# Kernel tuning notes

Measured on AMD Instinct MI355X. Metric: run time of the kernel, lower is better.

Reference implementation:

```python
import jax, jax.numpy as jnp
import numpy as np

N_EXPERTS = 8
TOPK = 2
W_IMPORTANCE = 0.01
W_LOAD = 0.01
LAMBDA_Z = 0.001
W_PENALTY = 0.01
PENALTY_TEMP = 1.66


def setup_inputs() -> dict:
    key = jax.random.key(0)
    ks = jax.random.split(key, 8)
    B, S, D, H, E = 8, 4096, 512, 2048, N_EXPERTS
    T = B * S
    return {
        "x": jax.random.normal(ks[0], (B, S, D), dtype=jnp.float32),
        "gate_w": jax.random.normal(ks[1], (E, D), dtype=jnp.float32) * 0.02,
        "noise_w": jax.random.normal(ks[2], (E, D), dtype=jnp.float32) * 0.02,
        "bias": jnp.zeros((E,), dtype=jnp.float32),
        "c_fc_w": jax.random.normal(ks[3], (E, H, D), dtype=jnp.float32) * 0.02,
        "c_fc_b": jnp.zeros((E, H), dtype=jnp.float32),
        "c_proj_w": jax.random.normal(ks[4], (E, D, H), dtype=jnp.float32) * 0.02,
        "c_proj_b": jnp.zeros((E, D), dtype=jnp.float32),
        "noise": jax.random.normal(ks[5], (T, E), dtype=jnp.float32),
    }


def reference(x, gate_w, noise_w, bias, c_fc_w, c_fc_b, c_proj_w, c_proj_b, noise):
    E, K = N_EXPERTS, TOPK
    D = x.shape[-1]
    xs = x.reshape(-1, D)                      # [T, D]
    T = xs.shape[0]

    gate_logits = xs @ gate_w.T                # [T, E]

    # penalty (pre-noise logits)
    p = jax.nn.softmax(gate_logits / PENALTY_TEMP, axis=-1)
    penalty_a = jnp.mean(p * (1.0 - p))
    pm = p.mean(axis=0)
    penalty_b = 1.0 / E - jnp.mean(pm * (1.0 - pm))
    penalty = (penalty_a + penalty_b) * W_PENALTY

    # z-loss (pre-noise logits)
    lse = jax.scipy.special.logsumexp(gate_logits, axis=-1)
    z_loss = LAMBDA_Z * jnp.mean(lse ** 2)

    # noisy gating + bias
    noise_std = jax.nn.softplus(xs @ noise_w.T)
    gate_logits = gate_logits + noise * noise_std + bias

    weights_vals, selected = jax.lax.top_k(gate_logits, K)   # [T, K]
    weights = jax.nn.softmax(weights_vals.astype(jnp.float32), axis=1).astype(x.dtype)

    # importance loss: scatter-add weights per expert
    importance = jax.ops.segment_sum(weights.reshape(-1), selected.reshape(-1),
                                     num_segments=E)
    cv2 = jnp.var(importance) / jnp.mean(importance) ** 2
    importance_loss = W_IMPORTANCE * cv2

    # load loss: top-1 counts vs mean router probs (post-noise)
    router_probs = jax.nn.softmax(gate_logits.astype(jnp.float32), axis=-1).astype(x.dtype)
    top1 = selected[:, 0]
    fi = jax.ops.segment_sum(jnp.ones((T,), dtype=jnp.float32), top1,
                             num_segments=E) / T
    load_loss = W_LOAD * E * jnp.sum(fi * router_probs.mean(axis=0))

    aux = penalty + z_loss + importance_loss + load_loss

    # combine weights per (token, expert): [T, E]
    comb = jnp.zeros((T, E), dtype=x.dtype).at[jnp.arange(T)[:, None], selected].add(weights)

    results = jnp.zeros_like(xs)
    for e in range(E):  # fixed small expert count
        h = jax.nn.gelu(xs @ c_fc_w[e].T + c_fc_b[e], approximate=True)
        o = h @ c_proj_w[e].T + c_proj_b[e]
        results = results + comb[:, e:e + 1] * o

    return results.reshape(x.shape), aux
```

## Files before the change

### kernel.cpp

```cpp
#include <hip/hip_runtime.h>
#include <hip/hip_bf16.h>
#include <stdint.h>

#define TTOK 32768
#define DDIM 512
#define HDIM 2048
#define NEXP 8
#define SBLK 128
#define IDXS (TTOK + 256)

typedef __attribute__((ext_vector_type(4))) float f32x4;
typedef __attribute__((ext_vector_type(8))) short bf16x8;

#define GLOAD16(gp, lp)                                                      \
  __builtin_amdgcn_global_load_lds(                                          \
      (const __attribute__((address_space(1))) unsigned int*)(gp),           \
      (__attribute__((address_space(3))) unsigned int*)(lp), 16, 0, 0)

__device__ __forceinline__ ushort f2bf(float f) {
  union { float f; uint32_t u; } cv; cv.f = f;
  uint32_t u = cv.u;
  u = u + 0x7fffu + ((u >> 16) & 1u);
  return (ushort)(u >> 16);
}

__device__ __forceinline__ float bf2f(ushort u) {
  union { uint32_t u; float f; } cv; cv.u = ((uint32_t)u) << 16;
  return cv.f;
}

__device__ __forceinline__ float gelu_fast(float v) {
  float y = 1.5957691216057308f * (v + 0.044715f * v * v * v);
  return v / (1.0f + __expf(-y));
}

__global__ __launch_bounds__(256) void cvtw2_kernel(
    const float* __restrict__ srcA, const float* __restrict__ srcB,
    ushort* __restrict__ dstA, ushort* __restrict__ dstB, int n4each) {
  int i = blockIdx.x * blockDim.x + threadIdx.x;
  const float* s;
  ushort* d;
  int j;
  if (i < n4each) { s = srcA; d = dstA; j = i; }
  else { j = i - n4each; if (j >= n4each) return; s = srcB; d = dstB; }
  float4 v = reinterpret_cast<const float4*>(s)[j];
  ushort4 o;
  o.x = f2bf(v.x); o.y = f2bf(v.y); o.z = f2bf(v.z); o.w = f2bf(v.w);
  reinterpret_cast<ushort4*>(d)[j] = o;
}

__global__ __launch_bounds__(256, 2) void gating1_kernel(
    const float* __restrict__ x, const float* __restrict__ gw,
    const float* __restrict__ nw, ushort* __restrict__ xbf,
    float* __restrict__ logits) {
  __shared__ float xs[16][516];
  __shared__ float wsm[16][516];
  const int tid = threadIdx.x;
  const int t0 = blockIdx.x * 16;

  for (int i = tid; i < 2048; i += 256) {
    int row = i >> 7;
    int d4 = (i & 127) << 2;
    const float* src = (row < 8) ? (gw + row * DDIM + d4)
                                 : (nw + (row - 8) * DDIM + d4);
    *reinterpret_cast<float4*>(&wsm[row][d4]) =
        *reinterpret_cast<const float4*>(src);
  }
  for (int i = tid; i < 2048; i += 256) {
    int row = i >> 7;
    int d4 = (i & 127) << 2;
    float4 v = *reinterpret_cast<const float4*>(x + (size_t)(t0 + row) * DDIM + d4);
    *reinterpret_cast<float4*>(&xs[row][d4]) = v;
    ushort4 u;
    u.x = f2bf(v.x); u.y = f2bf(v.y); u.z = f2bf(v.z); u.w = f2bf(v.w);
    *reinterpret_cast<ushort4*>(xbf + (size_t)(t0 + row) * DDIM + d4) = u;
  }
  __syncthreads();

  const int unit = tid & 15;
  const int tok = tid >> 4;
  const float* xr = &xs[tok][0];
  const float* wr = &wsm[unit][0];
  float a0 = 0.f, a1 = 0.f, a2 = 0.f, a3 = 0.f;
#pragma unroll 16
  for (int d = 0; d < 512; d += 4) {
    float4 xv = *reinterpret_cast<const float4*>(xr + d);
    float4 wv = *reinterpret_cast<const float4*>(wr + d);
    a0 = fmaf(xv.x, wv.x, a0);
    a1 = fmaf(xv.y, wv.y, a1);
    a2 = fmaf(xv.z, wv.z, a2);
    a3 = fmaf(xv.w, wv.w, a3);
  }
  logits[(size_t)(t0 + tok) * 16 + unit] = (a0 + a1) + (a2 + a3);
}

__global__ void gating2_kernel(
    const float* __restrict__ logits, const float* __restrict__ noise,
    const float* __restrict__ bias, int* __restrict__ cnt,
    int* __restrict__ idxl, int2* __restrict__ slots,
    float2* __restrict__ tokw, float* __restrict__ part) {
  const int tid = threadIdx.x;
  const int lane = tid & 63, wave = tid >> 6;
  const int t = blockIdx.x * 256 + tid;

  const float4* lp = reinterpret_cast<const float4*>(logits + (size_t)t * 16);
  float4 l0 = lp[0], l1 = lp[1], l2 = lp[2], l3 = lp[3];
  float lg[NEXP] = {l0.x, l0.y, l0.z, l0.w, l1.x, l1.y, l1.z, l1.w};
  float nl[NEXP] = {l2.x, l2.y, l2.z, l2.w, l3.x, l3.y, l3.z, l3.w};
  const float4* np = reinterpret_cast<const float4*>(noise + (size_t)t * NEXP);
  float4 z0 = np[0], z1 = np[1];
  float nz[NEXP] = {z0.x, z0.y, z0.z, z0.w, z1.x, z1.y, z1.z, z1.w};
  float bia[NEXP];
#pragma unroll
  for (int e = 0; e < NEXP; ++e) bia[e] = bias[e];

  float pa = 0.f, pm[NEXP];
  {
    float sv[NEXP];
#pragma unroll
    for (int e = 0; e < NEXP; ++e) sv[e] = lg[e] * (1.0f / 1.66f);
    float mx = sv[0];
#pragma unroll
    for (int e = 1; e < NEXP; ++e) mx = fmaxf(mx, sv[e]);
    float ssum = 0.f, pv[NEXP];
#pragma unroll
    for (int e = 0; e < NEXP; ++e) { pv[e] = __expf(sv[e] - mx); ssum += pv[e]; }
    float sinv = 1.f / ssum;
#pragma unroll
    for (int e = 0; e < NEXP; ++e) {
      float pe = pv[e] * sinv;
      pa += pe * (1.f - pe);
      pm[e] = pe;
    }
  }
  float z2;
  {
    float mg = lg[0];
#pragma unroll
    for (int e = 1; e < NEXP; ++e) mg = fmaxf(mg, lg[e]);
    float es = 0.f;
#pragma unroll
    for (int e = 0; e < NEXP; ++e) es += __expf(lg[e] - mg);
    float lse = mg + __logf(es);
    z2 = lse * lse;
  }
  float g2[NEXP];
#pragma unroll
  for (int e = 0; e < NEXP; ++e) {
    float s = nl[e];
    float sp = fmaxf(s, 0.f) + __logf(1.f + __expf(-fabsf(s)));
    g2[e] = lg[e] + nz[e] * sp + bia[e];
  }
  float v1 = g2[0]; int i1 = 0;
#pragma unroll
  for (int e = 1; e < NEXP; ++e) if (g2[e] > v1) { v1 = g2[e]; i1 = e; }
  float v2 = -3.4e38f; int i2 = 0;
#pragma unroll
  for (int e = 0; e < NEXP; ++e) if (e != i1 && g2[e] > v2) { v2 = g2[e]; i2 = e; }
  float dd = __expf(v2 - v1);
  float w1 = 1.f / (1.f + dd);
  float w2 = dd / (1.f + dd);
  float rp[NEXP];
  {
    float mr = g2[0];
#pragma unroll
    for (int e = 1; e < NEXP; ++e) mr = fmaxf(mr, g2[e]);
    float rs = 0.f, er[NEXP];
#pragma unroll
    for (int e = 0; e < NEXP; ++e) { er[e] = __expf(g2[e] - mr); rs += er[e]; }
    float rinv = 1.f / rs;
#pragma unroll
    for (int e = 0; e < NEXP; ++e) rp[e] = er[e] * rinv;
  }

  float loc[34];
  loc[0] = pa; loc[1] = z2;
#pragma unroll
  for (int e = 0; e < NEXP; ++e) {
    loc[2 + e]  = pm[e];
    loc[10 + e] = (e == i1 ? w1 : 0.f) + (e == i2 ? w2 : 0.f);
    loc[18 + e] = rp[e];
    loc[26 + e] = (e == i1) ? 1.f : 0.f;
  }
#pragma unroll
  for (int m = 1; m < 64; m <<= 1) {
#pragma unroll
    for (int s = 0; s < 34; ++s) loc[s] += __shfl_xor(loc[s], m);
  }
  __shared__ float red[4][34];
  if (lane == 0) {
#pragma unroll
    for (int s = 0; s < 34; ++s) red[wave][s] = loc[s];
  }
  __shared__ int lcnt[NEXP], gbase[NEXP];
  if (tid < NEXP) lcnt[tid] = 0;
  __syncthreads();
  int p1 = atomicAdd(&lcnt[i1], 1);
  int p2 = atomicAdd(&lcnt[i2], 1);
  __syncthreads();
  if (tid < NEXP) gbase[tid] = atomicAdd(&cnt[tid], lcnt[tid]);
  if (tid < 34) {
    float s = red[0][tid] + red[1][tid] + red[2][tid] + red[3][tid];
    part[(size_t)tid * SBLK + blockIdx.x] = s;
  }
  __syncthreads();
  int q1 = gbase[i1] + p1, q2 = gbase[i2] + p2;
  idxl[i1 * IDXS + q1] = t;
  idxl[i2 * IDXS + q2] = t;
  slots[t] = make_int2((i1 << 16) | q1, (i2 << 16) | q2);
  tokw[t] = make_float2(w1, w2);
}

__global__ __launch_bounds__(256) void finalize_kernel(
    const float* __restrict__ part, const int* __restrict__ cnt,
    int* __restrict__ offs, int* __restrict__ idxl,
    float* __restrict__ aux_out) {
  __shared__ float sums[34];
  __shared__ float red[4][34];
  __shared__ int roundc[NEXP], base[NEXP];
  const int tid = threadIdx.x;
  const int lane = tid & 63, wave = tid >> 6;

  float loc[34];
#pragma unroll
  for (int s = 0; s < 34; ++s) loc[s] = 0.f;
  for (int b = tid; b < SBLK; b += 256) {
#pragma unroll
    for (int s = 0; s < 34; ++s) loc[s] += part[(size_t)s * SBLK + b];
  }
#pragma unroll
  for (int m = 1; m < 64; m <<= 1) {
#pragma unroll
    for (int s = 0; s < 34; ++s) loc[s] += __shfl_xor(loc[s], m);
  }
  if (lane == 0) {
#pragma unroll
    for (int s = 0; s < 34; ++s) red[wave][s] = loc[s];
  }
  if (tid == 0) {
    int acc = 0;
    for (int e = 0; e < NEXP; ++e) {
      int r = (cnt[e] + 255) & ~255;
      roundc[e] = r; base[e] = acc; acc += r;
    }
  }
  __syncthreads();
  if (tid < 34) sums[tid] = red[0][tid] + red[1][tid] + red[2][tid] + red[3][tid];
  __syncthreads();
  for (int i = tid; i < NEXP * 256; i += 256) {
    int e = i >> 8, k = i & 255;
    int pos = cnt[e] + k;
    if (pos < roundc[e]) idxl[e * IDXS + pos] = 0;
  }
  if (tid < NEXP) offs[tid] = base[tid];
  if (tid == 0) {
    const float Tf = (float)TTOK;
    float pa = sums[0] / (Tf * 8.f);
    float pbm = 0.f;
    for (int e = 0; e < NEXP; ++e) { float pm = sums[2 + e] / Tf; pbm += pm * (1.f - pm); }
    float pb = 1.f / 8.f - pbm / 8.f;
    float penalty = (pa + pb) * 0.01f;
    float z = 0.001f * sums[1] / Tf;
    float mean = 0.f;
    for (int e = 0; e < NEXP; ++e) mean += sums[10 + e];
    mean /= 8.f;
    float var = 0.f;
    for (int e = 0; e < NEXP; ++e) { float d = sums[10 + e] - mean; var += d * d; }
    var /= 8.f;
    float il = 0.01f * var / (mean * mean);
    float ld = 0.f;
    for (int e = 0; e < NEXP; ++e) ld += (sums[26 + e] / Tf) * (sums[18 + e] / Tf);
    ld *= 0.01f * 8.f;
    aux_out[0] = penalty + z + il + ld;
  }
}


__global__ __launch_bounds__(512, 4) void gemm1_kernel(
    const ushort* __restrict__ xbf, const ushort* __restrict__ wfc,
    const float* __restrict__ fcb, const int* __restrict__ idxl,
    const int* __restrict__ cnt, const int* __restrict__ offs,
    ushort* __restrict__ h, int hbase, int HC) {
  const int e = blockIdx.z;
  const int count = cnt[e];
  const int rounded = (count + 255) & ~255;
  const int mt = blockIdx.x;
  if (mt * 256 >= rounded) return;
  const int nt = blockIdx.y;
  const int tid = threadIdx.x;
  const int lane = tid & 63, wave = tid >> 6;
  const int wm = wave >> 1, wn = wave & 1;

  __shared__ ushort As[256][64];
  __shared__ ushort Bs[128][64];

  const int srow = tid >> 3;
  const int csw8 = (((tid & 7) ^ (srow & 7)) << 3);
  const int dst8 = ((tid & 7) << 3);

  const ushort* aptr[4];
#pragma unroll
  for (int r = 0; r < 4; ++r) {
    int g = idxl[e * IDXS + mt * 256 + srow + r * 64];
    aptr[r] = xbf + (size_t)g * DDIM + csw8;
  }
  const ushort* bptr = wfc + (size_t)e * (HDIM * DDIM) +
                       (size_t)(hbase + nt * 128 + srow) * DDIM + csw8;

  f32x4 acc[4][4];
#pragma unroll
  for (int m = 0; m < 4; ++m)
#pragma unroll
    for (int n = 0; n < 4; ++n)
      acc[m][n] = (f32x4){0.f, 0.f, 0.f, 0.f};

  const int NK = DDIM / 64;
  for (int kt = 0; kt < NK; ++kt) {
    const int koff = kt * 64;
#pragma unroll
    for (int r = 0; r < 4; ++r)
      GLOAD16(aptr[r] + koff, &As[srow + r * 64][dst8]);
#pragma unroll
    for (int r = 0; r < 2; ++r)
      GLOAD16(bptr + (size_t)(r * 64) * DDIM + koff, &Bs[srow + r * 64][dst8]);
    asm volatile("s_waitcnt vmcnt(0)" ::: "memory");
    __syncthreads();
#pragma unroll
    for (int ks = 0; ks < 2; ++ks) {
      const int ch = (((ks << 2) | (lane >> 4)) ^ (lane & 7)) << 3;
      bf16x8 af[4], bfr[4];
#pragma unroll
      for (int m = 0; m < 4; ++m)
        af[m] = *reinterpret_cast<const bf16x8*>(&As[wm * 64 + m * 16 + (lane & 15)][ch]);
#pragma unroll
      for (int n = 0; n < 4; ++n)
        bfr[n] = *reinterpret_cast<const bf16x8*>(&Bs[wn * 64 + n * 16 + (lane & 15)][ch]);
#pragma unroll
      for (int m = 0; m < 4; ++m)
#pragma unroll
        for (int n = 0; n < 4; ++n)
          acc[m][n] = __builtin_amdgcn_mfma_f32_16x16x32_bf16(af[m], bfr[n], acc[m][n], 0, 0, 0);
    }
    __syncthreads();
  }

  const int hb = offs[e];
#pragma unroll
  for (int n = 0; n < 4; ++n) {
    const int col = wn * 64 + n * 16 + (lane & 15);
    const int gcol = hbase + nt * 128 + col;
    const float bterm = fcb[e * HDIM + gcol];
#pragma unroll
    for (int m = 0; m < 4; ++m) {
#pragma unroll
      for (int j = 0; j < 4; ++j) {
        const int row = mt * 256 + wm * 64 + m * 16 + ((lane >> 4) << 2) + j;
        float v = acc[m][n][j] + bterm;
        h[(size_t)(hb + row) * HC + (nt * 128 + col)] = f2bf(gelu_fast(v));
      }
    }
  }
}

__global__ __launch_bounds__(512, 4) void gemm2_kernel(
    const ushort* __restrict__ h, const ushort* __restrict__ wpj,
    const float* __restrict__ pjb, const int* __restrict__ cnt,
    const int* __restrict__ offs, ushort* __restrict__ scratch,
    int hbase, int HC, int first_chunk) {
  const int e = blockIdx.z;
  const int count = cnt[e];
  const int rounded = (count + 255) & ~255;
  const int mt = blockIdx.x;
  if (mt * 256 >= rounded) return;
  const int nt = blockIdx.y;
  const int tid = threadIdx.x;
  const int lane = tid & 63, wave = tid >> 6;
  const int wm = wave >> 1, wn = wave & 1;

  __shared__ ushort As[256][64];
  __shared__ ushort Bs[128][64];

  const int srow = tid >> 3;
  const int csw8 = (((tid & 7) ^ (srow & 7)) << 3);
  const int dst8 = ((tid & 7) << 3);
  const int hb = offs[e];

  const ushort* abase = h + (size_t)(hb + mt * 256 + srow) * HC + csw8;
  const ushort* bbase = wpj + (size_t)e * (DDIM * HDIM) +
                        (size_t)(nt * 128 + srow) * HDIM + hbase + csw8;

  f32x4 acc[4][4];
#pragma unroll
  for (int m = 0; m < 4; ++m)
#pragma unroll
    for (int n = 0; n < 4; ++n)
      acc[m][n] = (f32x4){0.f, 0.f, 0.f, 0.f};

  const int NK = HC / 64;
  for (int kt = 0; kt < NK; ++kt) {
    const int koff = kt * 64;
#pragma unroll
    for (int r = 0; r < 4; ++r)
      GLOAD16(abase + (size_t)(r * 64) * HC + koff, &As[srow + r * 64][dst8]);
#pragma unroll
    for (int r = 0; r < 2; ++r)
      GLOAD16(bbase + (size_t)(r * 64) * HDIM + koff, &Bs[srow + r * 64][dst8]);
    asm volatile("s_waitcnt vmcnt(0)" ::: "memory");
    __syncthreads();
#pragma unroll
    for (int ks = 0; ks < 2; ++ks) {
      const int ch = (((ks << 2) | (lane >> 4)) ^ (lane & 7)) << 3;
      bf16x8 af[4], bfr[4];
#pragma unroll
      for (int m = 0; m < 4; ++m)
        af[m] = *reinterpret_cast<const bf16x8*>(&As[wm * 64 + m * 16 + (lane & 15)][ch]);
#pragma unroll
      for (int n = 0; n < 4; ++n)
        bfr[n] = *reinterpret_cast<const bf16x8*>(&Bs[wn * 64 + n * 16 + (lane & 15)][ch]);
#pragma unroll
      for (int m = 0; m < 4; ++m)
#pragma unroll
        for (int n = 0; n < 4; ++n)
          acc[m][n] = __builtin_amdgcn_mfma_f32_16x16x32_bf16(af[m], bfr[n], acc[m][n], 0, 0, 0);
    }
    __syncthreads();
  }

#pragma unroll
  for (int n = 0; n < 4; ++n) {
    const int col = nt * 128 + wn * 64 + n * 16 + (lane & 15);
    const float bterm = pjb[e * DDIM + col];
#pragma unroll
    for (int m = 0; m < 4; ++m) {
#pragma unroll
      for (int j = 0; j < 4; ++j) {
        const size_t row = (size_t)(hb + mt * 256 + wm * 64 + m * 16 + ((lane >> 4) << 2) + j);
        ushort* p = scratch + row * DDIM + col;
        float v = acc[m][n][j];
        if (first_chunk) v += bterm;
        else v += bf2f(*p);
        *p = f2bf(v);
      }
    }
  }
}

__global__ __launch_bounds__(256, 8) void combine_kernel(
    const ushort* __restrict__ scratch, const int* __restrict__ offs,
    const int2* __restrict__ slots, const float2* __restrict__ tokw,
    float* __restrict__ out) {
  const int lane = threadIdx.x & 63;
  const int wave = threadIdx.x >> 6;
  const int t = blockIdx.x * 4 + wave;
  int2 s = slots[t];
  float2 w = tokw[t];
  const int r1 = offs[s.x >> 16] + (s.x & 0xFFFF);
  const int r2 = offs[s.y >> 16] + (s.y & 0xFFFF);
  bf16x8 a = *reinterpret_cast<const bf16x8*>(scratch + (size_t)r1 * DDIM + lane * 8);
  bf16x8 b = *reinterpret_cast<const bf16x8*>(scratch + (size_t)r2 * DDIM + lane * 8);
  float r[8];
#pragma unroll
  for (int j = 0; j < 8; ++j)
    r[j] = w.x * bf2f((ushort)a[j]) + w.y * bf2f((ushort)b[j]);
  float4* op = reinterpret_cast<float4*>(out + (size_t)t * DDIM + lane * 8);
  op[0] = make_float4(r[0], r[1], r[2], r[3]);
  op[1] = make_float4(r[4], r[5], r[6], r[7]);
}

extern "C" void kernel_launch(void* const* d_in, const int* in_sizes, int n_in,
                              void* d_out, int out_size, void* d_ws, size_t ws_size,
                              hipStream_t stream) {
  const float* x    = (const float*)d_in[0];
  const float* gw   = (const float*)d_in[1];
  const float* nw   = (const float*)d_in[2];
  const float* bias = (const float*)d_in[3];
  const float* fcw  = (const float*)d_in[4];
  const float* fcb  = (const float*)d_in[5];
  const float* pjw  = (const float*)d_in[6];
  const float* pjb  = (const float*)d_in[7];
  const float* noise = (const float*)d_in[8];
  float* out = (float*)d_out;

  char* ws = (char*)d_ws;
  size_t o = 0;
  auto alloc = [&](size_t bytes) -> char* {
    char* p = ws + o;
    o += (bytes + 255) & ~(size_t)255;
    return p;
  };
  ushort* xbf    = (ushort*)alloc((size_t)TTOK * DDIM * 2);
  ushort* wfcb   = (ushort*)alloc((size_t)NEXP * HDIM * DDIM * 2);
  ushort* wpjb   = (ushort*)alloc((size_t)NEXP * DDIM * HDIM * 2);
  float*  logits = (float*)alloc((size_t)TTOK * 16 * 4);
  int*    idxl   = (int*)alloc((size_t)NEXP * IDXS * 4);
  int2*   slots  = (int2*)alloc((size_t)TTOK * 8);
  float2* tokw   = (float2*)alloc((size_t)TTOK * 8);
  int*    cnt    = (int*)alloc(256);
  int*    offs   = (int*)alloc(256);
  float*  part   = (float*)alloc(34 * SBLK * 4);
  ushort* scr    = (ushort*)alloc((size_t)(2 * TTOK + 2048) * DDIM * 2);
  size_t fixed = o;

  int NCH = 16;
  const int chs[5] = {1, 2, 4, 8, 16};
  for (int ci = 0; ci < 5; ++ci) {
    size_t need = fixed + (size_t)(2 * TTOK + 2048) * (size_t)(HDIM / chs[ci]) * 2;
    if (need <= ws_size) { NCH = chs[ci]; break; }
  }
  const int HC = HDIM / NCH;
  ushort* h = (ushort*)alloc((size_t)(2 * TTOK + 2048) * HC * 2);

  hipMemsetAsync(cnt, 0, 32, stream);

  const int n4each = NEXP * HDIM * DDIM / 4;
  cvtw2_kernel<<<(2 * n4each + 255) / 256, 256, 0, stream>>>(fcw, pjw, wfcb, wpjb, n4each);
  gating1_kernel<<<TTOK / 16, 256, 0, stream>>>(x, gw, nw, xbf, logits);
  gating2_kernel<<<SBLK, 256, 0, stream>>>(logits, noise, bias, cnt, idxl, slots, tokw, part);
  finalize_kernel<<<1, 256, 0, stream>>>(part, cnt, offs, idxl, out + ((size_t)out_size - 1));

  for (int c = 0; c < NCH; ++c) {
    gemm1_kernel<<<dim3(128, HC / 128, NEXP), 512, 0, stream>>>(
        xbf, wfcb, fcb, idxl, cnt, offs, h, c * HC, HC);
    gemm2_kernel<<<dim3(128, 4, NEXP), 512, 0, stream>>>(
        h, wpjb, pjb, cnt, offs, scr, c * HC, HC, c == 0);
  }
  combine_kernel<<<TTOK / 4, 256, 0, stream>>>(scr, offs, slots, tokw, out);
}
```

Before: 695.0 us.

## Double-buffer A tiles in expert GEMMs to prefetch next K-slice during MFMA

Both expert GEMM kernels now hold two A tile buffers in LDS. The next A slice is issued via global_load_lds before the MFMA work on the current slice, while the B tile stays single-buffered and is reloaded after a barrier. The aim is to hide A-load latency behind compute. In exchange, LDS use per block grows from 48KB to 80KB, which may reduce occupancy below the launch-bounds target. There is also an exposed B-load wait each iteration, and the waitcnt(0) also waits on the A prefetch.

Measured after the change: 733.5 us. 1.06x slower.

```diff
diff --git a/kernel.cpp b/kernel.cpp
--- a/kernel.cpp
+++ b/kernel.cpp
@@ -291,7 +291,7 @@
   const int lane = tid & 63, wave = tid >> 6;
   const int wm = wave >> 1, wn = wave & 1;
 
-  __shared__ ushort As[256][64];
+  __shared__ ushort As[2][256][64];
   __shared__ ushort Bs[128][64];
 
   const int srow = tid >> 3;
@@ -314,24 +314,35 @@
     for (int n = 0; n < 4; ++n)
       acc[m][n] = (f32x4){0.f, 0.f, 0.f, 0.f};
 
+#define G1_ISSUE_A(buf, kt)                                                   \
+  {                                                                           \
+    const int koff = (kt) * 64;                                               \
+    _Pragma("unroll") for (int r = 0; r < 4; ++r)                             \
+      GLOAD16(aptr[r] + koff, &As[buf][srow + r * 64][dst8]);                 \
+  }
+#define G1_ISSUE_B(kt)                                                        \
+  {                                                                           \
+    const int koff = (kt) * 64;                                               \
+    _Pragma("unroll") for (int r = 0; r < 2; ++r)                             \
+      GLOAD16(bptr + (size_t)(r * 64) * DDIM + koff, &Bs[srow + r * 64][dst8]); \
+  }
+
+  G1_ISSUE_A(0, 0);
+  G1_ISSUE_B(0);
+  asm volatile("s_waitcnt vmcnt(0)" ::: "memory");
+  __builtin_amdgcn_s_barrier();
+
   const int NK = DDIM / 64;
   for (int kt = 0; kt < NK; ++kt) {
-    const int koff = kt * 64;
-#pragma unroll
-    for (int r = 0; r < 4; ++r)
-      GLOAD16(aptr[r] + koff, &As[srow + r * 64][dst8]);
-#pragma unroll
-    for (int r = 0; r < 2; ++r)
-      GLOAD16(bptr + (size_t)(r * 64) * DDIM + koff, &Bs[srow + r * 64][dst8]);
-    asm volatile("s_waitcnt vmcnt(0)" ::: "memory");
-    __syncthreads();
+    const int cur = kt & 1;
+    if (kt + 1 < NK) G1_ISSUE_A(cur ^ 1, kt + 1);
 #pragma unroll
     for (int ks = 0; ks < 2; ++ks) {
       const int ch = (((ks << 2) | (lane >> 4)) ^ (lane & 7)) << 3;
       bf16x8 af[4], bfr[4];
 #pragma unroll
       for (int m = 0; m < 4; ++m)
-        af[m] = *reinterpret_cast<const bf16x8*>(&As[wm * 64 + m * 16 + (lane & 15)][ch]);
+        af[m] = *reinterpret_cast<const bf16x8*>(&As[cur][wm * 64 + m * 16 + (lane & 15)][ch]);
 #pragma unroll
       for (int n = 0; n < 4; ++n)
         bfr[n] = *reinterpret_cast<const bf16x8*>(&Bs[wn * 64 + n * 16 + (lane & 15)][ch]);
@@ -341,7 +352,12 @@
         for (int n = 0; n < 4; ++n)
           acc[m][n] = __builtin_amdgcn_mfma_f32_16x16x32_bf16(af[m], bfr[n], acc[m][n], 0, 0, 0);
     }
-    __syncthreads();
+    __builtin_amdgcn_s_barrier();
+    if (kt + 1 < NK) {
+      G1_ISSUE_B(kt + 1);
+      asm volatile("s_waitcnt vmcnt(0)" ::: "memory");
+      __builtin_amdgcn_s_barrier();
+    }
   }
 
   const int hb = offs[e];
@@ -377,7 +393,7 @@
   const int lane = tid & 63, wave = tid >> 6;
   const int wm = wave >> 1, wn = wave & 1;
 
-  __shared__ ushort As[256][64];
+  __shared__ ushort As[2][256][64];
   __shared__ ushort Bs[128][64];
 
   const int srow = tid >> 3;
@@ -396,24 +412,35 @@
     for (int n = 0; n < 4; ++n)
       acc[m][n] = (f32x4){0.f, 0.f, 0.f, 0.f};
 
+#define G2_ISSUE_A(buf, kt)                                                   \
+  {                                                                           \
+    const int koff = (kt) * 64;                                               \
+    _Pragma("unroll") for (int r = 0; r < 4; ++r)                             \
+      GLOAD16(abase + (size_t)(r * 64) * HC + koff, &As[buf][srow + r * 64][dst8]); \
+  }
+#define G2_ISSUE_B(kt)                                                        \
+  {                                                                           \
+    const int koff = (kt) * 64;                                               \
+    _Pragma("unroll") for (int r = 0; r < 2; ++r)                             \
+      GLOAD16(bbase + (size_t)(r * 64) * HDIM + koff, &Bs[srow + r * 64][dst8]); \
+  }
+
+  G2_ISSUE_A(0, 0);
+  G2_ISSUE_B(0);
+  asm volatile("s_waitcnt vmcnt(0)" ::: "memory");
+  __builtin_amdgcn_s_barrier();
+
   const int NK = HC / 64;
   for (int kt = 0; kt < NK; ++kt) {
-    const int koff = kt * 64;
-#pragma unroll
-    for (int r = 0; r < 4; ++r)
-      GLOAD16(abase + (size_t)(r * 64) * HC + koff, &As[srow + r * 64][dst8]);
-#pragma unroll
-    for (int r = 0; r < 2; ++r)
-      GLOAD16(bbase + (size_t)(r * 64) * HDIM + koff, &Bs[srow + r * 64][dst8]);
-    asm volatile("s_waitcnt vmcnt(0)" ::: "memory");
-    __syncthreads();
+    const int cur = kt & 1;
+    if (kt + 1 < NK) G2_ISSUE_A(cur ^ 1, kt + 1);
 #pragma unroll
     for (int ks = 0; ks < 2; ++ks) {
       const int ch = (((ks << 2) | (lane >> 4)) ^ (lane & 7)) << 3;
       bf16x8 af[4], bfr[4];
 #pragma unroll
       for (int m = 0; m < 4; ++m)
-        af[m] = *reinterpret_cast<const bf16x8*>(&As[wm * 64 + m * 16 + (lane & 15)][ch]);
+        af[m] = *reinterpret_cast<const bf16x8*>(&As[cur][wm * 64 + m * 16 + (lane & 15)][ch]);
 #pragma unroll
       for (int n = 0; n < 4; ++n)
         bfr[n] = *reinterpret_cast<const bf16x8*>(&Bs[wn * 64 + n * 16 + (lane & 15)][ch]);
@@ -423,7 +450,12 @@
         for (int n = 0; n < 4; ++n)
           acc[m][n] = __builtin_amdgcn_mfma_f32_16x16x32_bf16(af[m], bfr[n], acc[m][n], 0, 0, 0);
     }
-    __syncthreads();
+    __builtin_amdgcn_s_barrier();
+    if (kt + 1 < NK) {
+      G2_ISSUE_B(kt + 1);
+      asm volatile("s_waitcnt vmcnt(0)" ::: "memory");
+      __builtin_amdgcn_s_barrier();
+    }
   }
 
 #pragma unroll
```
